# Optimization experiments

Hardware: AMD Instinct MI355X
Metric: run time of the kernel (lower is better)

## Reference

```python
import jax, jax.numpy as jnp
import numpy as np

DIM = 64


def setup_inputs() -> dict:
    key = jax.random.key(0)
    k1, k2, k3 = jax.random.split(key, 3)
    x = jax.random.normal(k1, (65536, DIM), dtype=jnp.float32)
    alpha = jax.random.uniform(k2, (), dtype=jnp.float32)
    beta = jax.random.uniform(k3, (), dtype=jnp.float32)
    return {"x": x, "alpha": alpha, "beta": beta}


def reference(x, alpha, beta):
    # Static upper-triangular index pairs (i < j), same as triu(...,1).nonzero()
    iu, ju = jnp.triu_indices(DIM, k=1)
    e = jnp.exp(-alpha * x)                 # [B, dim]
    # a[b, p] = exp(-alpha*x_i) - exp(-alpha*x_j) for each pair p=(i,j), i<j.
    # Equivalent to building the dense [B, dim, dim] tensor and gathering triu.
    a = e[..., iu] - e[..., ju]             # [B, dim*(dim-1)/2]
    log_vander = jnp.sum(jnp.log(jnp.abs(a)), axis=-1)  # [B]
    return 2.0 * (-beta * jnp.sum(x, axis=-1) + log_vander)
```

## Files before the change

### kernel.cpp

```cpp
#include <hip/hip_runtime.h>

#define DIM 64

__global__ __launch_bounds__(256) void vander_kernel(
    const float* __restrict__ x, const float* __restrict__ alpha,
    const float* __restrict__ beta, float* __restrict__ out, int nrows) {
  int row = blockIdx.x * blockDim.x + threadIdx.x;
  if (row >= nrows) return;

  const float c = -alpha[0] * 1.44269504088896340736f;
  const float b = beta[0];

  const float4* xr = reinterpret_cast<const float4*>(x) + row * (DIM / 4);

  float e[DIM];
  float xs = 0.f;
#pragma unroll
  for (int k = 0; k < DIM / 4; ++k) {
    float4 v = xr[k];
    xs += (v.x + v.y) + (v.z + v.w);
    e[4 * k + 0] = __builtin_amdgcn_exp2f(c * v.x);
    e[4 * k + 1] = __builtin_amdgcn_exp2f(c * v.y);
    e[4 * k + 2] = __builtin_amdgcn_exp2f(c * v.z);
    e[4 * k + 3] = __builtin_amdgcn_exp2f(c * v.w);
  }

  float accs[4] = {0.f, 0.f, 0.f, 0.f};
  float buf[4];
  int cnt = 0, g = 0;
#pragma unroll
  for (int i = 0; i < DIM; ++i) {
#pragma unroll
    for (int j = i + 1; j < DIM; ++j) {
      buf[cnt++] = e[i] - e[j];
      if (cnt == 4) {
        float p = (buf[0] * buf[1]) * (buf[2] * buf[3]);
        float ap = __builtin_fmaxf(__builtin_fabsf(p), 1e-37f);
        accs[g & 3] += __builtin_amdgcn_logf(ap);
        ++g;
        cnt = 0;
      }
    }
  }
  float lv = (accs[0] + accs[1]) + (accs[2] + accs[3]);
  out[row] = 2.0f * (-b * xs + 0.69314718055994530942f * lv);
}

extern "C" void kernel_launch(void* const* d_in, const int* in_sizes, int n_in,
                              void* d_out, int out_size, void* d_ws, size_t ws_size,
                              hipStream_t stream) {
  const float* x = (const float*)d_in[0];
  const float* alpha = (const float*)d_in[1];
  const float* beta = (const float*)d_in[2];
  float* out = (float*)d_out;
  int nrows = in_sizes[0] / DIM;
  int block = 256;
  int grid = (nrows + block - 1) / block;
  hipLaunchKernelGGL(vander_kernel, dim3(grid), dim3(block), 0, stream,
                     x, alpha, beta, out, nrows);
}
```

Baseline: 76.57 us.

## Split each row's pair products across eight waves via LDS-staged exponentials

Each block now handles 64 rows with 512 threads. Exponentials are computed cooperatively and staged in padded shared memory, and each of the eight waves computes one balanced share of the 2016 pair differences for every row. Products are grouped in eights, which halves the log calls compared with the previous groups of four. Per-wave partial sums are reduced through LDS. This removes the per-thread 64-float register array and the low parallelism of one thread per row. In exchange it adds LDS traffic, two barriers, and a greater risk of float overflow or underflow in the 8-term products.

```diff
diff --git a/kernel.cpp b/kernel.cpp
--- a/kernel.cpp
+++ b/kernel.cpp
@@ -1,49 +1,110 @@
 #include <hip/hip_runtime.h>
 
-#define DIM 64
+#define RS 66
 
-__global__ __launch_bounds__(256) void vander_kernel(
+__device__ __forceinline__ float lg8(float p) {
+  return __builtin_amdgcn_logf(__builtin_fmaxf(__builtin_fabsf(p), 1e-37f));
+}
+
+__device__ __forceinline__ void row8(float a, const float (&ej)[8], float& acc) {
+  float d0 = a - ej[0], d1 = a - ej[1], d2 = a - ej[2], d3 = a - ej[3];
+  float d4 = a - ej[4], d5 = a - ej[5], d6 = a - ej[6], d7 = a - ej[7];
+  acc += lg8(((d0 * d1) * (d2 * d3)) * ((d4 * d5) * (d6 * d7)));
+}
+
+__device__ __forceinline__ void ld8(const float* p, float (&r)[8]) {
+#pragma unroll
+  for (int k = 0; k < 4; ++k) {
+    float2 v = *reinterpret_cast<const float2*>(p + 2 * k);
+    r[2 * k] = v.x;
+    r[2 * k + 1] = v.y;
+  }
+}
+
+__device__ __forceinline__ void cross(const float (&ei)[8], const float (&ej)[8],
+                                      float& a0, float& a1) {
+  row8(ei[0], ej, a0); row8(ei[1], ej, a1);
+  row8(ei[2], ej, a0); row8(ei[3], ej, a1);
+  row8(ei[4], ej, a0); row8(ei[5], ej, a1);
+  row8(ei[6], ej, a0); row8(ei[7], ej, a1);
+}
+
+__device__ __forceinline__ void diag(const float (&e)[8], float& a0, float& a1) {
+  a0 += lg8((((e[0]-e[1])*(e[0]-e[2]))*((e[0]-e[3])*(e[0]-e[4]))) *
+            (((e[0]-e[5])*(e[0]-e[6]))*((e[0]-e[7])*(e[1]-e[2]))));
+  a1 += lg8((((e[1]-e[3])*(e[1]-e[4]))*((e[1]-e[5])*(e[1]-e[6]))) *
+            (((e[1]-e[7])*(e[2]-e[3]))*((e[2]-e[4])*(e[2]-e[5]))));
+  a0 += lg8((((e[2]-e[6])*(e[2]-e[7]))*((e[3]-e[4])*(e[3]-e[5]))) *
+            (((e[3]-e[6])*(e[3]-e[7]))*((e[4]-e[5])*(e[4]-e[6]))));
+  a1 += lg8(((e[4]-e[7])*(e[5]-e[6])) * ((e[5]-e[7])*(e[6]-e[7])));
+}
+
+__global__ __launch_bounds__(512, 8) void vander_kernel(
     const float* __restrict__ x, const float* __restrict__ alpha,
-    const float* __restrict__ beta, float* __restrict__ out, int nrows) {
-  int row = blockIdx.x * blockDim.x + threadIdx.x;
-  if (row >= nrows) return;
+    const float* __restrict__ beta, float* __restrict__ out) {
+  __shared__ float e_lds[64 * RS];
+  __shared__ float xsum[64 * 9];
+  __shared__ float ps[64 * 9];
 
+  const int tid = threadIdx.x;
   const float c = -alpha[0] * 1.44269504088896340736f;
-  const float b = beta[0];
 
-  const float4* xr = reinterpret_cast<const float4*>(x) + row * (DIM / 4);
+  {
+    const int r = tid >> 3, cc = tid & 7;
+    const float4* xp = reinterpret_cast<const float4*>(
+        x + ((size_t)blockIdx.x * 64 + r) * 64 + cc * 8);
+    float4 u = xp[0], v = xp[1];
+    float* ew = &e_lds[r * RS + cc * 8];
+    float2 t;
+    t.x = __builtin_amdgcn_exp2f(c * u.x); t.y = __builtin_amdgcn_exp2f(c * u.y);
+    *reinterpret_cast<float2*>(ew + 0) = t;
+    t.x = __builtin_amdgcn_exp2f(c * u.z); t.y = __builtin_amdgcn_exp2f(c * u.w);
+    *reinterpret_cast<float2*>(ew + 2) = t;
+    t.x = __builtin_amdgcn_exp2f(c * v.x); t.y = __builtin_amdgcn_exp2f(c * v.y);
+    *reinterpret_cast<float2*>(ew + 4) = t;
+    t.x = __builtin_amdgcn_exp2f(c * v.z); t.y = __builtin_amdgcn_exp2f(c * v.w);
+    *reinterpret_cast<float2*>(ew + 6) = t;
+    xsum[r * 9 + cc] = ((u.x + u.y) + (u.z + u.w)) + ((v.x + v.y) + (v.z + v.w));
+  }
+  __syncthreads();
 
-  float e[DIM];
-  float xs = 0.f;
-#pragma unroll
-  for (int k = 0; k < DIM / 4; ++k) {
-    float4 v = xr[k];
-    xs += (v.x + v.y) + (v.z + v.w);
-    e[4 * k + 0] = __builtin_amdgcn_exp2f(c * v.x);
-    e[4 * k + 1] = __builtin_amdgcn_exp2f(c * v.y);
-    e[4 * k + 2] = __builtin_amdgcn_exp2f(c * v.z);
-    e[4 * k + 3] = __builtin_amdgcn_exp2f(c * v.w);
+  const int lane = tid & 63;
+  const int w = tid >> 6;
+  const float* myrow = &e_lds[lane * RS];
+
+  float ei[8];
+  ld8(myrow + w * 8, ei);
+  float a0 = 0.f, a1 = 0.f;
+  float ej[8];
+
+  ld8(myrow + ((w + 1) & 7) * 8, ej);
+  cross(ei, ej, a0, a1);
+  ld8(myrow + ((w + 2) & 7) * 8, ej);
+  cross(ei, ej, a0, a1);
+  ld8(myrow + ((w + 3) & 7) * 8, ej);
+  cross(ei, ej, a0, a1);
+
+  ld8(myrow + ((w + 4) & 7) * 8, ej);
+  if (w < 4) {
+    row8(ei[0], ej, a0); row8(ei[1], ej, a1);
+    row8(ei[2], ej, a0); row8(ei[3], ej, a1);
+  } else {
+    row8(ej[4], ei, a0); row8(ej[5], ei, a1);
+    row8(ej[6], ei, a0); row8(ej[7], ei, a1);
   }
+  diag(ei, a0, a1);
 
-  float accs[4] = {0.f, 0.f, 0.f, 0.f};
-  float buf[4];
-  int cnt = 0, g = 0;
-#pragma unroll
-  for (int i = 0; i < DIM; ++i) {
-#pragma unroll
-    for (int j = i + 1; j < DIM; ++j) {
-      buf[cnt++] = e[i] - e[j];
-      if (cnt == 4) {
-        float p = (buf[0] * buf[1]) * (buf[2] * buf[3]);
-        float ap = __builtin_fmaxf(__builtin_fabsf(p), 1e-37f);
-        accs[g & 3] += __builtin_amdgcn_logf(ap);
-        ++g;
-        cnt = 0;
-      }
-    }
+  ps[lane * 9 + w] = a0 + a1;
+  __syncthreads();
+
+  if (w == 0) {
+    const float* pp = &ps[lane * 9];
+    const float* xq = &xsum[lane * 9];
+    float lv = ((pp[0] + pp[1]) + (pp[2] + pp[3])) + ((pp[4] + pp[5]) + (pp[6] + pp[7]));
+    float xs = ((xq[0] + xq[1]) + (xq[2] + xq[3])) + ((xq[4] + xq[5]) + (xq[6] + xq[7]));
+    out[blockIdx.x * 64 + lane] =
+        2.0f * (-beta[0] * xs + 0.69314718055994530942f * lv);
   }
-  float lv = (accs[0] + accs[1]) + (accs[2] + accs[3]);
-  out[row] = 2.0f * (-b * xs + 0.69314718055994530942f * lv);
 }
 
 extern "C" void kernel_launch(void* const* d_in, const int* in_sizes, int n_in,
@@ -53,9 +114,8 @@
   const float* alpha = (const float*)d_in[1];
   const float* beta = (const float*)d_in[2];
   float* out = (float*)d_out;
-  int nrows = in_sizes[0] / DIM;
-  int block = 256;
-  int grid = (nrows + block - 1) / block;
-  hipLaunchKernelGGL(vander_kernel, dim3(grid), dim3(block), 0, stream,
-                     x, alpha, beta, out, nrows);
+  int nrows = in_sizes[0] / 64;
+  int grid = nrows / 64;
+  hipLaunchKernelGGL(vander_kernel, dim3(grid), dim3(512), 0, stream,
+                     x, alpha, beta, out);
 }
```

Result: faster. 71.52 us (-6.6%).
